# Optimization experiments

Measured on AMD Instinct MI355X. Metric: run time of the kernel, lower is better.

The kernel has to match this reference:

```python
import jax, jax.numpy as jnp
import numpy as np

N_NODES = 100000
N_EDGES = 1000000
D_MODEL = 128
EDGE_DIM = 64
LN_EPS = 1e-5


def _layernorm(x, gamma, beta, eps=LN_EPS):
    mu = jnp.mean(x, axis=-1, keepdims=True)
    var = jnp.var(x, axis=-1, keepdims=True)
    return (x - mu) * jax.lax.rsqrt(var + eps) * gamma + beta


def setup_inputs() -> dict:
    key = jax.random.key(0)
    ks = jax.random.split(key, 12)
    std = 1.0 / np.sqrt(D_MODEL)
    stde = 1.0 / np.sqrt(EDGE_DIM)
    return {
        "x_src": jax.random.normal(ks[0], (N_NODES, D_MODEL), jnp.float32),
        "x_dst": jax.random.normal(ks[1], (N_NODES, D_MODEL), jnp.float32),
        "edge_attr": jax.random.normal(ks[2], (N_EDGES, EDGE_DIM), jnp.float32),
        "edge_index": jax.random.randint(ks[3], (2, N_EDGES), 0, N_NODES, jnp.int32),
        # params
        "W_src": jax.random.uniform(ks[4], (D_MODEL, D_MODEL), jnp.float32, -std, std),
        "W_dst": jax.random.uniform(ks[5], (D_MODEL, D_MODEL), jnp.float32, -std, std),
        "b_dst": jnp.zeros((D_MODEL,), jnp.float32),
        "Wg1": jax.random.uniform(ks[6], (EDGE_DIM, D_MODEL), jnp.float32, -stde, stde),
        "bg1": jnp.zeros((D_MODEL,), jnp.float32),
        "Wg2": jax.random.uniform(ks[7], (D_MODEL, 1), jnp.float32, -std, std),
        "bg2": jnp.zeros((1,), jnp.float32),
        "gamma": jnp.ones((D_MODEL,), jnp.float32),
        "beta": jnp.zeros((D_MODEL,), jnp.float32),
    }


def reference(x_src, x_dst, edge_attr, edge_index,
              W_src, W_dst, b_dst, Wg1, bg1, Wg2, bg2, gamma, beta):
    s, d = edge_index[0], edge_index[1]
    n = x_dst.shape[0]
    # gather + linear (no bias): [E, D]
    msg = x_src[s] @ W_src
    # edge gate MLP: Linear -> gelu -> Linear (no norm, eval so no dropout)
    h = jax.nn.gelu(edge_attr @ Wg1 + bg1, approximate=False)
    gate = jax.nn.sigmoid(h @ Wg2 + bg2)  # [E, 1]
    msg = msg * gate
    # scatter-add aggregate + mean by in-degree (clamped at 1)
    out = jax.ops.segment_sum(msg, d, num_segments=n)
    deg = jax.ops.segment_sum(jnp.ones((msg.shape[0],), msg.dtype), d, num_segments=n)
    out = out / jnp.clip(deg, 1.0)[:, None]
    # residual-like combine, layernorm, gelu
    out = _layernorm(out + x_dst @ W_dst + b_dst, gamma, beta)
    return jax.nn.gelu(out, approximate=False)
```

## Files before the change

### kernel.cpp

```cpp
#include <hip/hip_runtime.h>
#include <hip/hip_fp16.h>
#include <math.h>

#define N_NODES 100000
#define N_EDGES 1000000
#define D_MODEL 128
#define EDGE_DIM 64
#define SCHUNK 250
#define NSB 400

typedef short bf16x8 __attribute__((ext_vector_type(8)));
typedef float f32x4 __attribute__((ext_vector_type(4)));
typedef float f32x2 __attribute__((ext_vector_type(2)));

__device__ __forceinline__ short f2bf(float f) {
    union { float f; unsigned u; } v; v.f = f;
    unsigned r = v.u + 0x7FFFu + ((v.u >> 16) & 1u);
    return (short)(r >> 16);
}
__device__ __forceinline__ float gelu_fast(float x) {
    float t = 0.7978845608028654f * x * (1.0f + 0.044715f * x * x);
    float e = __expf(2.0f * t);
    return x * (1.0f - __builtin_amdgcn_rcpf(e + 1.0f));
}
__device__ __forceinline__ float sigmoid_fast(float x) {
    return __builtin_amdgcn_rcpf(1.0f + __expf(-x));
}
__device__ __forceinline__ float bflo(unsigned v) { return __uint_as_float(v << 16); }
__device__ __forceinline__ float bfhi(unsigned v) { return __uint_as_float(v & 0xFFFF0000u); }
__device__ __forceinline__ bf16x8 cvt8(float4 v0, float4 v1) {
    bf16x8 t;
    t[0] = f2bf(v0.x); t[1] = f2bf(v0.y); t[2] = f2bf(v0.z); t[3] = f2bf(v0.w);
    t[4] = f2bf(v1.x); t[5] = f2bf(v1.y); t[6] = f2bf(v1.z); t[7] = f2bf(v1.w);
    return t;
}

#if __has_builtin(__builtin_amdgcn_cvt_pk_fp8_f32) && __has_builtin(__builtin_amdgcn_cvt_pk_f32_fp8)
__device__ __forceinline__ unsigned char fp8_enc(float f) {
    int p = __builtin_amdgcn_cvt_pk_fp8_f32(f, f, 0, false);
    return (unsigned char)(p & 0xFF);
}
template <bool HI>
__device__ __forceinline__ f32x2 fp8_dec2(unsigned dw) {
    return __builtin_amdgcn_cvt_pk_f32_fp8((int)dw, HI);
}
#else
__device__ __forceinline__ unsigned char fp8_enc(float f) {
    unsigned su = (__float_as_uint(f) >> 24) & 0x80u;
    float af = fminf(fabsf(f), 448.0f);
    unsigned u = __float_as_uint(af);
    int e = (int)((u >> 23) & 255) - 120;
    unsigned b;
    if (e <= 0) b = (unsigned)__float2int_rn(af * 512.0f);
    else {
        unsigned m = (u >> 20) & 7u;
        unsigned rnd = (u >> 19) & 1u;
        b = (((unsigned)e << 3) | m) + rnd;
    }
    b = min(b, 126u);
    return (unsigned char)(su | b);
}
__device__ __forceinline__ float fp8d1(unsigned b) {
    unsigned s = (b & 0x80u) << 24;
    unsigned em = b & 0x7Fu;
    float mag;
    if (em >= 8) mag = __uint_as_float((((em >> 3) + 120u) << 23) | ((em & 7u) << 20));
    else mag = (float)em * 0.001953125f;
    return __uint_as_float(s | __float_as_uint(mag));
}
template <bool HI>
__device__ __forceinline__ f32x2 fp8_dec2(unsigned dw) {
    unsigned w = HI ? (dw >> 16) : dw;
    f32x2 r; r[0] = fp8d1(w & 0xFFu); r[1] = fp8d1((w >> 8) & 0xFFu);
    return r;
}
#endif

__global__ __launch_bounds__(256) void k_prep(
    const float* __restrict__ Ws, const float* __restrict__ Wd,
    const float* __restrict__ Wg1, short* __restrict__ frag,
    int* __restrict__ deg)
{
    int b = blockIdx.x;
    if (b >= 20) {
        int i = (b - 20) * 256 + threadIdx.x;
        if (i < N_NODES) deg[i] = 0;
        return;
    }
    int g = b * 256 + threadIdx.x;
    if (g >= 5120) return;
    const float* W; short* T; int q;
    if (g < 2048)      { W = Ws;  T = frag;         q = g; }
    else if (g < 4096) { W = Wd;  T = frag + 16384; q = g - 2048; }
    else               { W = Wg1; T = frag + 32768; q = g - 4096; }
    int ls = q & 63, nt = (q >> 6) & 7, kb = q >> 9;
    int col = nt * 16 + (ls & 15);
    int k0 = kb * 32 + (ls >> 4) * 8;
    bf16x8 v;
    #pragma unroll
    for (int e = 0; e < 8; ++e) v[e] = f2bf(W[(k0 + e) * D_MODEL + col]);
    *reinterpret_cast<bf16x8*>(T + (size_t)q * 8) = v;
}

__global__ void k_deg(const int* __restrict__ dst, int* __restrict__ deg, int* __restrict__ rank) {
    int e = blockIdx.x * 256 + threadIdx.x;
    if (e < N_EDGES) rank[e] = atomicAdd(&deg[dst[e]], 1);
}

__global__ __launch_bounds__(256) void k_scan1(const int* __restrict__ deg, int* __restrict__ bsum) {
    __shared__ int s[256];
    int tid = threadIdx.x;
    int i = blockIdx.x * SCHUNK + tid;
    int v = (tid < SCHUNK && i < N_NODES) ? deg[i] : 0;
    s[tid] = v; __syncthreads();
    for (int off = 128; off > 0; off >>= 1) {
        if (tid < off) s[tid] += s[tid + off];
        __syncthreads();
    }
    if (tid == 0) bsum[blockIdx.x] = s[0];
}
__global__ __launch_bounds__(512) void k_scan2(const int* __restrict__ bsum, int* __restrict__ boff) {
    __shared__ int s[512];
    int tid = threadIdx.x;
    int v = (tid < NSB) ? bsum[tid] : 0;
    s[tid] = v; __syncthreads();
    for (int off = 1; off < 512; off <<= 1) {
        int t = (tid >= off) ? s[tid - off] : 0;
        __syncthreads();
        s[tid] += t;
        __syncthreads();
    }
    if (tid < NSB) boff[tid] = s[tid] - v;
}
__global__ __launch_bounds__(256) void k_scan3(const int* __restrict__ deg, const int* __restrict__ boff,
                                               int* __restrict__ rstart) {
    __shared__ int s[256];
    int tid = threadIdx.x;
    int i = blockIdx.x * SCHUNK + tid;
    int v = (tid < SCHUNK && i < N_NODES) ? deg[i] : 0;
    s[tid] = v; __syncthreads();
    for (int off = 1; off < 256; off <<= 1) {
        int t = (tid >= off) ? s[tid - off] : 0;
        __syncthreads();
        s[tid] += t;
        __syncthreads();
    }
    int excl = s[tid] - v;
    if (tid < SCHUNK && i < N_NODES) {
        rstart[i] = boff[blockIdx.x] + excl;
        if (i == N_NODES - 1) rstart[N_NODES] = boff[blockIdx.x] + excl + v;
    }
}

__global__ __launch_bounds__(256, 3) void k_node_linear(
    const float* __restrict__ x_src, const float* __restrict__ x_dst,
    const short* __restrict__ WsrcF, const short* __restrict__ WdstF,
    const float* __restrict__ b_dst,
    unsigned char* __restrict__ ysrc, short* __restrict__ z_bf)
{
    __shared__ __align__(16) short Bf[4][8][64][8];
    const int tid = threadIdx.x;
    const int lane = tid & 63;
    const int wid = tid >> 6;
    const int l15 = lane & 15;
    const int lg = lane >> 4;
    const int mat = blockIdx.y;
    const float* __restrict__ X = mat ? x_dst : x_src;
    const short* __restrict__ WF = mat ? WdstF : WsrcF;
    const int row0 = blockIdx.x * 128 + wid * 32;

    const float* rowp[2];
    #pragma unroll
    for (int st = 0; st < 2; ++st) {
        int r = min(row0 + st * 16 + l15, N_NODES - 1);
        rowp[st] = X + (size_t)r * D_MODEL + lg * 8;
    }

    float4 buf[2][2][2];
    #pragma unroll
    for (int st = 0; st < 2; ++st) {
        buf[0][st][0] = *reinterpret_cast<const float4*>(rowp[st]);
        buf[0][st][1] = *reinterpret_cast<const float4*>(rowp[st] + 4);
    }

    #pragma unroll
    for (int i = 0; i < 8; ++i)
        reinterpret_cast<int4*>(Bf)[tid + i * 256] =
            reinterpret_cast<const int4*>(WF)[tid + i * 256];

    f32x4 acc[2][8];
    #pragma unroll
    for (int st = 0; st < 2; ++st)
        #pragma unroll
        for (int nt = 0; nt < 8; ++nt) { f32x4 zz = {0.f,0.f,0.f,0.f}; acc[st][nt] = zz; }

    __syncthreads();

    #pragma unroll
    for (int kb = 0; kb < 4; ++kb) {
        if (kb < 3) {
            #pragma unroll
            for (int st = 0; st < 2; ++st) {
                buf[(kb + 1) & 1][st][0] = *reinterpret_cast<const float4*>(rowp[st] + (kb + 1) * 32);
                buf[(kb + 1) & 1][st][1] = *reinterpret_cast<const float4*>(rowp[st] + (kb + 1) * 32 + 4);
            }
        }
        bf16x8 a[2];
        #pragma unroll
        for (int st = 0; st < 2; ++st)
            a[st] = cvt8(buf[kb & 1][st][0], buf[kb & 1][st][1]);
        #pragma unroll
        for (int nt = 0; nt < 8; ++nt) {
            bf16x8 b = *reinterpret_cast<const bf16x8*>(&Bf[kb][nt][lane][0]);
            acc[0][nt] = __builtin_amdgcn_mfma_f32_16x16x32_bf16(a[0], b, acc[0][nt], 0, 0, 0);
            acc[1][nt] = __builtin_amdgcn_mfma_f32_16x16x32_bf16(a[1], b, acc[1][nt], 0, 0, 0);
        }
    }

    #pragma unroll
    for (int st = 0; st < 2; ++st) {
        int rowb = row0 + st * 16 + lg * 4;
        #pragma unroll
        for (int nt = 0; nt < 8; ++nt) {
            int col = nt * 16 + l15;
            float bias = mat ? b_dst[col] : 0.0f;
            #pragma unroll
            for (int r = 0; r < 4; ++r) {
                int row = rowb + r;
                if (row < N_NODES) {
                    float v = acc[st][nt][r];
                    if (mat) z_bf[(size_t)row * D_MODEL + col] = f2bf(v + bias);
                    else     ysrc[(size_t)row * D_MODEL + col] = fp8_enc(v);
                }
            }
        }
    }
}

__global__ __launch_bounds__(256, 5) void k_gate_fill(
    const float* __restrict__ ea, const short* __restrict__ Wg1F,
    const float* __restrict__ bg1, const float* __restrict__ Wg2,
    const float* __restrict__ bg2,
    const int* __restrict__ dstI, const int* __restrict__ srcI,
    const int* __restrict__ rank, const int* __restrict__ rstart,
    int2* __restrict__ sg)
{
    __shared__ __align__(16) short Bf[2][8][64][8];
    const int tid = threadIdx.x;
    const int lane = tid & 63;
    const int wid = tid >> 6;
    const int l15 = lane & 15;
    const int lg = lane >> 4;
    const int e0 = blockIdx.x * 128 + wid * 32;

    const float* rp[2];
    #pragma unroll
    for (int st = 0; st < 2; ++st) {
        int r = min(e0 + st * 16 + l15, N_EDGES - 1);
        rp[st] = ea + (size_t)r * EDGE_DIM + lg * 8;
    }
    float4 b0[2][2];
    #pragma unroll
    for (int st = 0; st < 2; ++st) {
        b0[st][0] = *reinterpret_cast<const float4*>(rp[st]);
        b0[st][1] = *reinterpret_cast<const float4*>(rp[st] + 4);
    }
    #pragma unroll
    for (int i = 0; i < 4; ++i)
        reinterpret_cast<int4*>(Bf)[tid + i * 256] =
            reinterpret_cast<const int4*>(Wg1F)[tid + i * 256];
    float4 b1[2][2];
    #pragma unroll
    for (int st = 0; st < 2; ++st) {
        b1[st][0] = *reinterpret_cast<const float4*>(rp[st] + 32);
        b1[st][1] = *reinterpret_cast<const float4*>(rp[st] + 36);
    }
    __syncthreads();

    bf16x8 aA[2], aB[2];
    #pragma unroll
    for (int st = 0; st < 2; ++st) aA[st] = cvt8(b0[st][0], b0[st][1]);
    #pragma unroll
    for (int st = 0; st < 2; ++st) aB[st] = cvt8(b1[st][0], b1[st][1]);

    float part[2][4] = {{0.f,0.f,0.f,0.f},{0.f,0.f,0.f,0.f}};
    #pragma unroll
    for (int ntc = 0; ntc < 2; ++ntc) {
        f32x4 acc[2][4];
        #pragma unroll
        for (int st = 0; st < 2; ++st)
            #pragma unroll
            for (int nt = 0; nt < 4; ++nt) { f32x4 zz = {0.f,0.f,0.f,0.f}; acc[st][nt] = zz; }
        #pragma unroll
        for (int nt = 0; nt < 4; ++nt) {
            bf16x8 b = *reinterpret_cast<const bf16x8*>(&Bf[0][ntc * 4 + nt][lane][0]);
            acc[0][nt] = __builtin_amdgcn_mfma_f32_16x16x32_bf16(aA[0], b, acc[0][nt], 0, 0, 0);
            acc[1][nt] = __builtin_amdgcn_mfma_f32_16x16x32_bf16(aA[1], b, acc[1][nt], 0, 0, 0);
        }
        #pragma unroll
        for (int nt = 0; nt < 4; ++nt) {
            bf16x8 b = *reinterpret_cast<const bf16x8*>(&Bf[1][ntc * 4 + nt][lane][0]);
            acc[0][nt] = __builtin_amdgcn_mfma_f32_16x16x32_bf16(aB[0], b, acc[0][nt], 0, 0, 0);
            acc[1][nt] = __builtin_amdgcn_mfma_f32_16x16x32_bf16(aB[1], b, acc[1][nt], 0, 0, 0);
        }
        #pragma unroll
        for (int nt = 0; nt < 4; ++nt) {
            int col = (ntc * 4 + nt) * 16 + l15;
            float b1c = bg1[col];
            float w2 = Wg2[col];
            #pragma unroll
            for (int st = 0; st < 2; ++st)
                #pragma unroll
                for (int r = 0; r < 4; ++r)
                    part[st][r] += gelu_fast(acc[st][nt][r] + b1c) * w2;
        }
    }

    #pragma unroll
    for (int m = 1; m <= 8; m <<= 1)
        #pragma unroll
        for (int st = 0; st < 2; ++st)
            #pragma unroll
            for (int r = 0; r < 4; ++r)
                part[st][r] += __shfl_xor(part[st][r], m);

    if (l15 == 0) {
        float b2 = bg2[0];
        #pragma unroll
        for (int st = 0; st < 2; ++st)
            #pragma unroll
            for (int r = 0; r < 4; ++r) {
                int e = e0 + st * 16 + lg * 4 + r;
                if (e < N_EDGES) {
                    float gv = sigmoid_fast(part[st][r] + b2);
                    int d = dstI[e];
                    int p = rstart[d] + rank[e];
                    int2 v; v.x = srcI[e]; v.y = __float_as_int(gv);
                    sg[p] = v;
                }
            }
    }
}

__global__ __launch_bounds__(256) void k_agg(
    const int* __restrict__ rstart, const int2* __restrict__ sg,
    const unsigned char* __restrict__ ysrc, const short* __restrict__ z_bf,
    const float* __restrict__ gamma, const float* __restrict__ beta,
    float* __restrict__ out)
{
    const int lane = threadIdx.x & 63;
    const int wid = threadIdx.x >> 6;
    const int n = blockIdx.x * 4 + wid;
    const int l15 = lane & 15;
    const int lg = lane >> 4;
    const int d0 = l15 * 8;
    const int start = rstart[n];
    const int end = rstart[n + 1];
    const int dg = end - start;

    uint4 zv = *reinterpret_cast<const uint4*>(&z_bf[(size_t)n * D_MODEL + d0]);
    float4 gA = *reinterpret_cast<const float4*>(&gamma[d0]);
    float4 gB = *reinterpret_cast<const float4*>(&gamma[d0 + 4]);
    float4 bA = *reinterpret_cast<const float4*>(&beta[d0]);
    float4 bB = *reinterpret_cast<const float4*>(&beta[d0 + 4]);

    float a[8];
    #pragma unroll
    for (int j = 0; j < 8; ++j) a[j] = 0.f;

    int t = start + lg;
    bool v = t < end;
    int2 eC = make_int2(0, 0); uint2 pC = make_uint2(0, 0);
    if (v) {
        eC = sg[t];
        pC = *reinterpret_cast<const uint2*>(&ysrc[(size_t)eC.x * D_MODEL + d0]);
    }
    while (v) {
        int t2 = t + 4;
        bool v2 = t2 < end;
        int2 eN = make_int2(0, 0); uint2 pN = make_uint2(0, 0);
        if (v2) {
            eN = sg[t2];
            pN = *reinterpret_cast<const uint2*>(&ysrc[(size_t)eN.x * D_MODEL + d0]);
        }
        float g = __int_as_float(eC.y);
        f32x2 q0 = fp8_dec2<false>(pC.x);
        f32x2 q1 = fp8_dec2<true>(pC.x);
        f32x2 q2 = fp8_dec2<false>(pC.y);
        f32x2 q3 = fp8_dec2<true>(pC.y);
        a[0] += g * q0[0]; a[1] += g * q0[1];
        a[2] += g * q1[0]; a[3] += g * q1[1];
        a[4] += g * q2[0]; a[5] += g * q2[1];
        a[6] += g * q3[0]; a[7] += g * q3[1];
        t = t2; eC = eN; pC = pN; v = v2;
    }

    #pragma unroll
    for (int j = 0; j < 8; ++j) {
        a[j] += __shfl_xor(a[j], 16);
        a[j] += __shfl_xor(a[j], 32);
    }

    float inv = 1.0f / fmaxf((float)dg, 1.0f);
    float tv[8];
    tv[0] = a[0] * inv + bflo(zv.x); tv[1] = a[1] * inv + bfhi(zv.x);
    tv[2] = a[2] * inv + bflo(zv.y); tv[3] = a[3] * inv + bfhi(zv.y);
    tv[4] = a[4] * inv + bflo(zv.z); tv[5] = a[5] * inv + bfhi(zv.z);
    tv[6] = a[6] * inv + bflo(zv.w); tv[7] = a[7] * inv + bfhi(zv.w);

    float s = 0.f;
    #pragma unroll
    for (int j = 0; j < 8; ++j) s += tv[j];
    #pragma unroll
    for (int m = 1; m <= 8; m <<= 1) s += __shfl_xor(s, m);
    float mu = s * (1.0f / 128.0f);

    float vs = 0.f;
    float dv[8];
    #pragma unroll
    for (int j = 0; j < 8; ++j) { dv[j] = tv[j] - mu; vs += dv[j] * dv[j]; }
    #pragma unroll
    for (int m = 1; m <= 8; m <<= 1) vs += __shfl_xor(vs, m);
    float rstd = rsqrtf(vs * (1.0f / 128.0f) + 1e-5f);

    float o[8];
    o[0] = gelu_fast(dv[0] * rstd * gA.x + bA.x);
    o[1] = gelu_fast(dv[1] * rstd * gA.y + bA.y);
    o[2] = gelu_fast(dv[2] * rstd * gA.z + bA.z);
    o[3] = gelu_fast(dv[3] * rstd * gA.w + bA.w);
    o[4] = gelu_fast(dv[4] * rstd * gB.x + bB.x);
    o[5] = gelu_fast(dv[5] * rstd * gB.y + bB.y);
    o[6] = gelu_fast(dv[6] * rstd * gB.z + bB.z);
    o[7] = gelu_fast(dv[7] * rstd * gB.w + bB.w);

    if (lg == 0) {
        float4 w = make_float4(o[0], o[1], o[2], o[3]);
        *reinterpret_cast<float4*>(&out[(size_t)n * D_MODEL + d0]) = w;
    } else if (lg == 1) {
        float4 w = make_float4(o[4], o[5], o[6], o[7]);
        *reinterpret_cast<float4*>(&out[(size_t)n * D_MODEL + d0 + 4]) = w;
    }
}

extern "C" void kernel_launch(void* const* d_in, const int* in_sizes, int n_in,
                              void* d_out, int out_size, void* d_ws, size_t ws_size,
                              hipStream_t stream)
{
    const float* x_src = (const float*)d_in[0];
    const float* x_dst = (const float*)d_in[1];
    const float* ea    = (const float*)d_in[2];
    const int*   ei    = (const int*)d_in[3];
    const float* W_src = (const float*)d_in[4];
    const float* W_dst = (const float*)d_in[5];
    const float* b_dst = (const float*)d_in[6];
    const float* Wg1   = (const float*)d_in[7];
    const float* bg1   = (const float*)d_in[8];
    const float* Wg2   = (const float*)d_in[9];
    const float* bg2   = (const float*)d_in[10];
    const float* gamma = (const float*)d_in[11];
    const float* beta  = (const float*)d_in[12];
    const int* srcIdx = ei;
    const int* dstIdx = ei + N_EDGES;

    char* ws = (char*)d_ws;
    short*         fragT  = (short*)(ws);
    unsigned char* ysrc   = (unsigned char*)(ws + 81920);
    short*         z_bf   = (short*)(ws + 12881920);
    int*           deg    = (int*)(ws + 38481920);
    int*           rank   = (int*)(ws + 38881920);
    int*           rstart = (int*)(ws + 42881920);
    int2*          sg     = (int2*)(ws + 43281928);
    int*           bsum   = (int*)(ws + 51281928);
    int*           boff   = (int*)(ws + 51283528);

    float* out = (float*)d_out;

    hipLaunchKernelGGL(k_prep, dim3(411), dim3(256), 0, stream, W_src, W_dst, Wg1, fragT, deg);
    hipLaunchKernelGGL(k_deg, dim3(3907), dim3(256), 0, stream, dstIdx, deg, rank);
    hipLaunchKernelGGL(k_scan1, dim3(NSB), dim3(256), 0, stream, deg, bsum);
    hipLaunchKernelGGL(k_scan2, dim3(1), dim3(512), 0, stream, bsum, boff);
    hipLaunchKernelGGL(k_scan3, dim3(NSB), dim3(256), 0, stream, deg, boff, rstart);
    hipLaunchKernelGGL(k_node_linear, dim3(782, 2), dim3(256), 0, stream,
                       x_src, x_dst, fragT, fragT + 16384, b_dst, ysrc, z_bf);
    hipLaunchKernelGGL(k_gate_fill, dim3(7813), dim3(256), 0, stream,
                       ea, fragT + 32768, bg1, Wg2, bg2, dstIdx, srcIdx, rank, rstart, sg);
    hipLaunchKernelGGL(k_agg, dim3(N_NODES / 4), dim3(256), 0, stream,
                       rstart, sg, ysrc, z_bf, gamma, beta, out);
}
```

Baseline: 251.0 us.

## Fuse node linear and edge gate kernels into one interleaved launch

Merges the node-linear GEMM kernel and the edge-gate/fill kernel into a single launch. Every sixth block runs a node-linear tile and the other five run gate tiles, so the two independent workloads run on the GPU at the same time. This removes one launch and the idle tail between the two kernels. In exchange the fused kernel takes the larger shared-memory footprint and the combined register pressure, and its launch bound changes from 5 to 4 blocks per CU for the gate path, which may lower occupancy.

```diff
diff --git a/kernel.cpp b/kernel.cpp
--- a/kernel.cpp
+++ b/kernel.cpp
@@ -8,6 +8,8 @@
 #define EDGE_DIM 64
 #define SCHUNK 250
 #define NSB 400
+#define NL_BLOCKS 1564
+#define GATE_BLOCKS 7813
 
 typedef short bf16x8 __attribute__((ext_vector_type(8)));
 typedef float f32x4 __attribute__((ext_vector_type(4)));
@@ -152,106 +154,108 @@
     }
 }
 
-__global__ __launch_bounds__(256, 3) void k_node_linear(
+__global__ __launch_bounds__(256, 4) void k_fused_main(
     const float* __restrict__ x_src, const float* __restrict__ x_dst,
-    const short* __restrict__ WsrcF, const short* __restrict__ WdstF,
-    const float* __restrict__ b_dst,
-    unsigned char* __restrict__ ysrc, short* __restrict__ z_bf)
-{
-    __shared__ __align__(16) short Bf[4][8][64][8];
-    const int tid = threadIdx.x;
-    const int lane = tid & 63;
-    const int wid = tid >> 6;
-    const int l15 = lane & 15;
-    const int lg = lane >> 4;
-    const int mat = blockIdx.y;
-    const float* __restrict__ X = mat ? x_dst : x_src;
-    const short* __restrict__ WF = mat ? WdstF : WsrcF;
-    const int row0 = blockIdx.x * 128 + wid * 32;
-
-    const float* rowp[2];
-    #pragma unroll
-    for (int st = 0; st < 2; ++st) {
-        int r = min(row0 + st * 16 + l15, N_NODES - 1);
-        rowp[st] = X + (size_t)r * D_MODEL + lg * 8;
-    }
-
-    float4 buf[2][2][2];
-    #pragma unroll
-    for (int st = 0; st < 2; ++st) {
-        buf[0][st][0] = *reinterpret_cast<const float4*>(rowp[st]);
-        buf[0][st][1] = *reinterpret_cast<const float4*>(rowp[st] + 4);
-    }
-
-    #pragma unroll
-    for (int i = 0; i < 8; ++i)
-        reinterpret_cast<int4*>(Bf)[tid + i * 256] =
-            reinterpret_cast<const int4*>(WF)[tid + i * 256];
-
-    f32x4 acc[2][8];
-    #pragma unroll
-    for (int st = 0; st < 2; ++st)
-        #pragma unroll
-        for (int nt = 0; nt < 8; ++nt) { f32x4 zz = {0.f,0.f,0.f,0.f}; acc[st][nt] = zz; }
-
-    __syncthreads();
-
-    #pragma unroll
-    for (int kb = 0; kb < 4; ++kb) {
-        if (kb < 3) {
-            #pragma unroll
-            for (int st = 0; st < 2; ++st) {
-                buf[(kb + 1) & 1][st][0] = *reinterpret_cast<const float4*>(rowp[st] + (kb + 1) * 32);
-                buf[(kb + 1) & 1][st][1] = *reinterpret_cast<const float4*>(rowp[st] + (kb + 1) * 32 + 4);
-            }
-        }
-        bf16x8 a[2];
-        #pragma unroll
-        for (int st = 0; st < 2; ++st)
-            a[st] = cvt8(buf[kb & 1][st][0], buf[kb & 1][st][1]);
-        #pragma unroll
-        for (int nt = 0; nt < 8; ++nt) {
-            bf16x8 b = *reinterpret_cast<const bf16x8*>(&Bf[kb][nt][lane][0]);
-            acc[0][nt] = __builtin_amdgcn_mfma_f32_16x16x32_bf16(a[0], b, acc[0][nt], 0, 0, 0);
-            acc[1][nt] = __builtin_amdgcn_mfma_f32_16x16x32_bf16(a[1], b, acc[1][nt], 0, 0, 0);
-        }
-    }
-
-    #pragma unroll
-    for (int st = 0; st < 2; ++st) {
-        int rowb = row0 + st * 16 + lg * 4;
-        #pragma unroll
-        for (int nt = 0; nt < 8; ++nt) {
-            int col = nt * 16 + l15;
-            float bias = mat ? b_dst[col] : 0.0f;
-            #pragma unroll
-            for (int r = 0; r < 4; ++r) {
-                int row = rowb + r;
-                if (row < N_NODES) {
-                    float v = acc[st][nt][r];
-                    if (mat) z_bf[(size_t)row * D_MODEL + col] = f2bf(v + bias);
-                    else     ysrc[(size_t)row * D_MODEL + col] = fp8_enc(v);
-                }
-            }
-        }
-    }
-}
-
-__global__ __launch_bounds__(256, 5) void k_gate_fill(
-    const float* __restrict__ ea, const short* __restrict__ Wg1F,
+    const short* __restrict__ fragT, const float* __restrict__ b_dst,
+    unsigned char* __restrict__ ysrc, short* __restrict__ z_bf,
+    const float* __restrict__ ea,
     const float* __restrict__ bg1, const float* __restrict__ Wg2,
     const float* __restrict__ bg2,
     const int* __restrict__ dstI, const int* __restrict__ srcI,
     const int* __restrict__ rank, const int* __restrict__ rstart,
     int2* __restrict__ sg)
 {
-    __shared__ __align__(16) short Bf[2][8][64][8];
+    __shared__ __align__(16) short Bf[4][8][64][8];
+    const int bid = blockIdx.x;
+    const int q6 = bid / 6;
+    const int r6 = bid - q6 * 6;
     const int tid = threadIdx.x;
     const int lane = tid & 63;
     const int wid = tid >> 6;
     const int l15 = lane & 15;
     const int lg = lane >> 4;
-    const int e0 = blockIdx.x * 128 + wid * 32;
+
+    if (r6 == 0) {
+        const int vb = q6;
+        const int mat = vb >= 782;
+        const int bx = mat ? vb - 782 : vb;
+        const float* __restrict__ X = mat ? x_dst : x_src;
+        const short* __restrict__ WF = mat ? fragT + 16384 : fragT;
+        const int row0 = bx * 128 + wid * 32;
+
+        const float* rowp[2];
+        #pragma unroll
+        for (int st = 0; st < 2; ++st) {
+            int r = min(row0 + st * 16 + l15, N_NODES - 1);
+            rowp[st] = X + (size_t)r * D_MODEL + lg * 8;
+        }
+
+        float4 buf[2][2][2];
+        #pragma unroll
+        for (int st = 0; st < 2; ++st) {
+            buf[0][st][0] = *reinterpret_cast<const float4*>(rowp[st]);
+            buf[0][st][1] = *reinterpret_cast<const float4*>(rowp[st] + 4);
+        }
+
+        #pragma unroll
+        for (int i = 0; i < 8; ++i)
+            reinterpret_cast<int4*>(Bf)[tid + i * 256] =
+                reinterpret_cast<const int4*>(WF)[tid + i * 256];
+
+        f32x4 acc[2][8];
+        #pragma unroll
+        for (int st = 0; st < 2; ++st)
+            #pragma unroll
+            for (int nt = 0; nt < 8; ++nt) { f32x4 zz = {0.f,0.f,0.f,0.f}; acc[st][nt] = zz; }
+
+        __syncthreads();
+
+        #pragma unroll
+        for (int kb = 0; kb < 4; ++kb) {
+            if (kb < 3) {
+                #pragma unroll
+                for (int st = 0; st < 2; ++st) {
+                    buf[(kb + 1) & 1][st][0] = *reinterpret_cast<const float4*>(rowp[st] + (kb + 1) * 32);
+                    buf[(kb + 1) & 1][st][1] = *reinterpret_cast<const float4*>(rowp[st] + (kb + 1) * 32 + 4);
+                }
+            }
+            bf16x8 a[2];
+            #pragma unroll
+            for (int st = 0; st < 2; ++st)
+                a[st] = cvt8(buf[kb & 1][st][0], buf[kb & 1][st][1]);
+            #pragma unroll
+            for (int nt = 0; nt < 8; ++nt) {
+                bf16x8 b = *reinterpret_cast<const bf16x8*>(&Bf[kb][nt][lane][0]);
+                acc[0][nt] = __builtin_amdgcn_mfma_f32_16x16x32_bf16(a[0], b, acc[0][nt], 0, 0, 0);
+                acc[1][nt] = __builtin_amdgcn_mfma_f32_16x16x32_bf16(a[1], b, acc[1][nt], 0, 0, 0);
+            }
+        }
+
+        #pragma unroll
+        for (int st = 0; st < 2; ++st) {
+            int rowb = row0 + st * 16 + lg * 4;
+            #pragma unroll
+            for (int nt = 0; nt < 8; ++nt) {
+                int col = nt * 16 + l15;
+                float bias = mat ? b_dst[col] : 0.0f;
+                #pragma unroll
+                for (int r = 0; r < 4; ++r) {
+                    int row = rowb + r;
+                    if (row < N_NODES) {
+                        float v = acc[st][nt][r];
+                        if (mat) z_bf[(size_t)row * D_MODEL + col] = f2bf(v + bias);
+                        else     ysrc[(size_t)row * D_MODEL + col] = fp8_enc(v);
+                    }
+                }
+            }
+        }
+        return;
+    }
+
+    const int gid = q6 * 5 + (r6 - 1);
+    if (gid >= GATE_BLOCKS) return;
+    const short* __restrict__ Wg1F = fragT + 32768;
+    const int e0 = gid * 128 + wid * 32;
 
     const float* rp[2];
     #pragma unroll
@@ -480,10 +484,9 @@
     hipLaunchKernelGGL(k_scan1, dim3(NSB), dim3(256), 0, stream, deg, bsum);
     hipLaunchKernelGGL(k_scan2, dim3(1), dim3(512), 0, stream, bsum, boff);
     hipLaunchKernelGGL(k_scan3, dim3(NSB), dim3(256), 0, stream, deg, boff, rstart);
-    hipLaunchKernelGGL(k_node_linear, dim3(782, 2), dim3(256), 0, stream,
-                       x_src, x_dst, fragT, fragT + 16384, b_dst, ysrc, z_bf);
-    hipLaunchKernelGGL(k_gate_fill, dim3(7813), dim3(256), 0, stream,
-                       ea, fragT + 32768, bg1, Wg2, bg2, dstIdx, srcIdx, rank, rstart, sg);
+    hipLaunchKernelGGL(k_fused_main, dim3(6 * NL_BLOCKS), dim3(256), 0, stream,
+                       x_src, x_dst, fragT, b_dst, ysrc, z_bf,
+                       ea, bg1, Wg2, bg2, dstIdx, srcIdx, rank, rstart, sg);
     hipLaunchKernelGGL(k_agg, dim3(N_NODES / 4), dim3(256), 0, stream,
                        rstart, sg, ysrc, z_bf, gamma, beta, out);
 }
```

Measured after the change: 274.7 us. 1.09x slower.
